# Performance work log

Hardware: AMD Instinct MI355X
Metric: run time of the kernel (lower is better)

The kernel has to match this reference:

```python
import jax, jax.numpy as jnp
import numpy as np

B, T, C, L = 256, 256, 1024, 64
NEG = jnp.float32(-1e30)  # finite stand-in for -inf (safe under exp)
EPS = 1e-7  # keras.backend.epsilon()


def setup_inputs() -> dict:
    key = jax.random.key(0)
    k1, k2 = jax.random.split(key)
    # y_pred: softmax-like probabilities (Keras ctc_batch_cost expects probs)
    y_pred = jax.random.uniform(k1, (B, T, C), dtype=jnp.float32)
    y_true = jax.random.randint(k2, (B, L), 0, C - 1, dtype=jnp.int64)  # blank = C-1 excluded
    return {"y_true": y_true, "y_pred": y_pred}


def reference(y_true, y_pred):
    # Faithful to keras.backend.ctc_batch_cost with input_length=T, label_length=L:
    # logits = log(y_pred + eps); tf.nn.ctc_loss applies log_softmax internally; blank = C-1.
    b, t, c = y_pred.shape
    l = y_true.shape[1]
    blank = c - 1
    logp = jax.nn.log_softmax(jnp.log(y_pred + EPS), axis=-1)  # [B,T,C]

    # Extended label sequence: blank, l1, blank, l2, ..., blank  (length S = 2L+1)
    s = 2 * l + 1
    ext = jnp.full((b, s), blank, dtype=y_true.dtype).at[:, 1::2].set(y_true)  # [B,S]
    pos = jnp.arange(s)
    prev2 = jnp.concatenate([jnp.full((b, 2), blank, dtype=ext.dtype), ext[:, :-2]], axis=1)
    # transition s-2 -> s allowed only for non-blank labels differing from label two back
    skip_ok = (ext != blank) & (ext != prev2) & (pos >= 2)  # [B,S]

    # Emission log-probs gathered at extended labels: [B,T,S]
    emit = jnp.take_along_axis(logp, jnp.broadcast_to(ext[:, None, :], (b, t, s)), axis=2)

    # Forward DP (log-space) over time via scan
    alpha0 = jnp.where(pos < 2, emit[:, 0, :], NEG)  # only states 0,1 reachable at t=0

    def step(alpha, emit_t):
        a1 = alpha
        a2 = jnp.concatenate([jnp.full((b, 1), NEG), alpha[:, :-1]], axis=1)
        a3 = jnp.where(skip_ok, jnp.concatenate([jnp.full((b, 2), NEG), alpha[:, :-2]], axis=1), NEG)
        m = jnp.maximum(a1, jnp.maximum(a2, a3))
        alpha_new = m + jnp.log(jnp.exp(a1 - m) + jnp.exp(a2 - m) + jnp.exp(a3 - m)) + emit_t
        return alpha_new, None

    alphaT, _ = jax.lax.scan(step, alpha0, jnp.swapaxes(emit, 0, 1)[1:])  # scan over T-1 steps

    tail = alphaT[:, s - 2:]  # valid end states: last label or final blank
    m = jnp.max(tail, axis=1)
    loglik = m + jnp.log(jnp.sum(jnp.exp(tail - m[:, None]), axis=1))
    return -loglik[:, None]  # [B,1], matches ctc_batch_cost output shape
```

## Files before the change

### kernel.cpp

```cpp
#include <hip/hip_runtime.h>
#include <hip/hip_bf16.h>


#define NEGF (-1e30f)

__device__ __forceinline__ float lse2(float a, float b) {
    float m = fmaxf(a, b);
    return m + log2f(exp2f(a - m) + exp2f(b - m));
}
__device__ __forceinline__ float lse3(float a, float b, float c) {
    float m = fmaxf(fmaxf(a, b), c);
    return m + log2f(exp2f(a - m) + exp2f(b - m) + exp2f(c - m));
}

__global__ void __launch_bounds__(256) emit_kernel(
    const float* __restrict__ y, const int* __restrict__ lab,
    float* __restrict__ lpl, float* __restrict__ lpb) {
    const int wave = threadIdx.x >> 6;
    const int lane = threadIdx.x & 63;
    const int row  = (blockIdx.x << 2) + wave;
    const int b    = row >> 8;
    const float* __restrict__ yr = y + ((size_t)row << 10);
    const float4* __restrict__ yr4 = (const float4*)yr;

    float4 v0 = yr4[lane];
    float4 v1 = yr4[lane + 64];
    float4 v2 = yr4[lane + 128];
    float4 v3 = yr4[lane + 192];
    float s = (v0.x + v0.y + v0.z + v0.w) + (v1.x + v1.y + v1.z + v1.w)
            + (v2.x + v2.y + v2.z + v2.w) + (v3.x + v3.y + v3.z + v3.w);
    #pragma unroll
    for (int off = 32; off; off >>= 1) s += __shfl_xor(s, off);

    const float norm = log2f(s + 1.024e-4f);

    const int c = lab[(b << 6) + lane];
    const float yv = yr[c];
    lpl[((size_t)row << 6) + lane] = log2f(yv + 1e-7f) - norm;
    if (lane == 0)
        lpb[row] = log2f(yr[1023] + 1e-7f) - norm;
}

__global__ void __launch_bounds__(64) ctc_alpha_kernel(
    const int* __restrict__ lab,
    const float* __restrict__ lpl, const float* __restrict__ lpb,
    float* __restrict__ out) {
    const int b    = blockIdx.x;
    const int lane = threadIdx.x;

    const int myLab   = lab[(b << 6) + lane];
    const int prevLab = __shfl_up(myLab, 1);
    const bool skip   = (lane >= 1) && (myLab != prevLab);

    const size_t rowbase = (size_t)b << 8;

    float eb = lpb[rowbase];
    float el = lpl[(rowbase << 6) + lane];
    float a0 = (lane == 0) ? eb : NEGF;
    float a1 = (lane == 0) ? el : NEGF;
    float a2 = NEGF;

    for (int t = 1; t < 256; ++t) {
        eb = lpb[rowbase + t];
        el = lpl[((rowbase + t) << 6) + lane];
        float p1 = __shfl_up(a1, 1);
        if (lane == 0) p1 = NEGF;
        float a1_63 = __shfl(a1, 63);
        float n0 = lse2(a0, p1) + eb;
        float n1 = lse3(a1, a0, skip ? p1 : NEGF) + el;
        float n2 = lse2(a2, a1_63) + eb;
        a0 = n0; a1 = n1; a2 = n2;
    }

    float t127 = __shfl(a1, 63);
    float ll = lse2(t127, a2);
    if (lane == 0)
        out[b] = -ll * 0.6931471805599453f;
}

extern "C" void kernel_launch(void* const* d_in, const int* in_sizes, int n_in,
                              void* d_out, int out_size, void* d_ws, size_t ws_size,
                              hipStream_t stream) {
    const int*   y_true = (const int*)d_in[0];
    const float* y_pred = (const float*)d_in[1];
    float* out = (float*)d_out;

    float* lpl = (float*)d_ws;
    float* lpb = lpl + (size_t)256 * 256 * 64;

    emit_kernel<<<16384, 256, 0, stream>>>(y_pred, y_true, lpl, lpb);
    ctc_alpha_kernel<<<256, 64, 0, stream>>>(y_true, lpl, lpb, out);
}
```

Measured before the change: 426.8 us.

## Fuse emission and alpha recursion into one kernel via shared memory

```diff
diff --git a/kernel.cpp b/kernel.cpp
--- a/kernel.cpp
+++ b/kernel.cpp
@@ -13,56 +13,53 @@
     return m + log2f(exp2f(a - m) + exp2f(b - m) + exp2f(c - m));
 }
 
-__global__ void __launch_bounds__(256) emit_kernel(
+__global__ void __launch_bounds__(1024) ctc_fused_kernel(
     const float* __restrict__ y, const int* __restrict__ lab,
-    float* __restrict__ lpl, float* __restrict__ lpb) {
+    float* __restrict__ out)
+{
+    __shared__ float lpl_s[256][64];
+    __shared__ float lpb_s[256];
+
+    const int b    = blockIdx.x;
     const int wave = threadIdx.x >> 6;
     const int lane = threadIdx.x & 63;
-    const int row  = (blockIdx.x << 2) + wave;
-    const int b    = row >> 8;
-    const float* __restrict__ yr = y + ((size_t)row << 10);
-    const float4* __restrict__ yr4 = (const float4*)yr;
 
-    float4 v0 = yr4[lane];
-    float4 v1 = yr4[lane + 64];
-    float4 v2 = yr4[lane + 128];
-    float4 v3 = yr4[lane + 192];
-    float s = (v0.x + v0.y + v0.z + v0.w) + (v1.x + v1.y + v1.z + v1.w)
-            + (v2.x + v2.y + v2.z + v2.w) + (v3.x + v3.y + v3.z + v3.w);
-    #pragma unroll
-    for (int off = 32; off; off >>= 1) s += __shfl_xor(s, off);
+    const int myLab = lab[(b << 6) + lane];
 
-    const float norm = log2f(s + 1.024e-4f);
+    for (int i = 0; i < 16; ++i) {
+        const int t = (wave << 4) + i;
+        const float* __restrict__ yr = y + ((size_t)(b * 256 + t) << 10);
+        const float4* __restrict__ yr4 = (const float4*)yr;
+        float4 v0 = yr4[lane];
+        float4 v1 = yr4[lane + 64];
+        float4 v2 = yr4[lane + 128];
+        float4 v3 = yr4[lane + 192];
+        float s = (v0.x + v0.y + v0.z + v0.w) + (v1.x + v1.y + v1.z + v1.w)
+                + (v2.x + v2.y + v2.z + v2.w) + (v3.x + v3.y + v3.z + v3.w);
+        #pragma unroll
+        for (int off = 32; off; off >>= 1) s += __shfl_xor(s, off);
+        const float norm = log2f(s + 1.024e-4f);
+        const float yv = yr[myLab];
+        lpl_s[t][lane] = log2f(yv + 1e-7f) - norm;
+        if (lane == 0)
+            lpb_s[t] = log2f(yr[1023] + 1e-7f) - norm;
+    }
+    __syncthreads();
 
-    const int c = lab[(b << 6) + lane];
-    const float yv = yr[c];
-    lpl[((size_t)row << 6) + lane] = log2f(yv + 1e-7f) - norm;
-    if (lane == 0)
-        lpb[row] = log2f(yr[1023] + 1e-7f) - norm;
-}
+    if (wave != 0) return;
 
-__global__ void __launch_bounds__(64) ctc_alpha_kernel(
-    const int* __restrict__ lab,
-    const float* __restrict__ lpl, const float* __restrict__ lpb,
-    float* __restrict__ out) {
-    const int b    = blockIdx.x;
-    const int lane = threadIdx.x;
-
-    const int myLab   = lab[(b << 6) + lane];
     const int prevLab = __shfl_up(myLab, 1);
     const bool skip   = (lane >= 1) && (myLab != prevLab);
 
-    const size_t rowbase = (size_t)b << 8;
-
-    float eb = lpb[rowbase];
-    float el = lpl[(rowbase << 6) + lane];
+    float eb = lpb_s[0];
+    float el = lpl_s[0][lane];
     float a0 = (lane == 0) ? eb : NEGF;
     float a1 = (lane == 0) ? el : NEGF;
     float a2 = NEGF;
 
     for (int t = 1; t < 256; ++t) {
-        eb = lpb[rowbase + t];
-        el = lpl[((rowbase + t) << 6) + lane];
+        eb = lpb_s[t];
+        el = lpl_s[t][lane];
         float p1 = __shfl_up(a1, 1);
         if (lane == 0) p1 = NEGF;
         float a1_63 = __shfl(a1, 63);
@@ -85,9 +82,5 @@
     const float* y_pred = (const float*)d_in[1];
     float* out = (float*)d_out;
 
-    float* lpl = (float*)d_ws;
-    float* lpb = lpl + (size_t)256 * 256 * 64;
-
-    emit_kernel<<<16384, 256, 0, stream>>>(y_pred, y_true, lpl, lpb);
-    ctc_alpha_kernel<<<256, 64, 0, stream>>>(y_true, lpl, lpb, out);
+    ctc_fused_kernel<<<256, 1024, 0, stream>>>(y_pred, y_true, out);
 }
```

After: 421.9 us. Within noise of the previous version (-1.2%).
